# Kernel tuning notes

Hardware: AMD Instinct MI355X
Metric: run time of the kernel (lower is better)

The kernel has to match this reference:

```python
import jax, jax.numpy as jnp
import numpy as np

# Production dims: NTU-RGB+D skeletons, mid-network AGCN block
N, C, T, V = 64, 64, 300, 25   # batch, channels, frames, joints
S = 3                          # num_subset (spatial partitions of adjacency)
IC = 64 // 4                   # inter_channels = out_channels // coff_embedding
OC = 64                        # out_channels (== in_channels -> down is Identity)
BN_EPS = 1e-5


def setup_inputs() -> dict:
    key = jax.random.key(0)
    ks = jax.random.split(key, 13)
    x = jax.random.normal(ks[0], (N, C, T, V), jnp.float32)
    A = jax.random.uniform(ks[1], (S, V, V), jnp.float32)          # fixed graph buffer
    PA = jax.random.normal(ks[2], (S, V, V), jnp.float32) * 1e-3   # learned adjacency (init ~1e-6)
    wa = jax.random.normal(ks[3], (S, IC, C), jnp.float32) * 0.05  # conv_a 1x1 weights
    ba = jax.random.normal(ks[4], (S, IC), jnp.float32) * 0.01
    wb = jax.random.normal(ks[5], (S, IC, C), jnp.float32) * 0.05  # conv_b 1x1 weights
    bb = jax.random.normal(ks[6], (S, IC), jnp.float32) * 0.01
    wd = jax.random.normal(ks[7], (S, OC, C), jnp.float32) * 0.05  # conv_d 1x1 weights
    bd = jax.random.normal(ks[8], (S, OC), jnp.float32) * 0.01
    bn_gamma = jax.random.uniform(ks[9], (OC,), jnp.float32) + 0.5
    bn_beta = jax.random.normal(ks[10], (OC,), jnp.float32) * 0.1
    bn_mean = jax.random.normal(ks[11], (OC,), jnp.float32) * 0.1
    bn_var = jax.random.uniform(ks[12], (OC,), jnp.float32) + 0.5
    return {"x": x, "A": A, "PA": PA, "wa": wa, "ba": ba, "wb": wb, "bb": bb,
            "wd": wd, "bd": bd, "bn_gamma": bn_gamma, "bn_beta": bn_beta,
            "bn_mean": bn_mean, "bn_var": bn_var}


def reference(x, A, PA, wa, ba, wb, bb, wd, bd, bn_gamma, bn_beta, bn_mean, bn_var):
    n, c, t, v = x.shape
    s, ic, _ = wa.shape
    A_total = A + PA                                                # (S,V,V)

    # conv_a / conv_b are 1x1 convs over channels, vectorized over subsets
    a = jnp.einsum('nctv,skc->nsktv', x, wa) + ba[None, :, :, None, None]  # (N,S,IC,T,V)
    b = jnp.einsum('nctv,skc->nsktv', x, wb) + bb[None, :, :, None, None]

    # attention_a: permute(0,3,1,2).view(N, V, IC*T); attention_b: view(N, IC*T, V)
    a_flat = a.transpose(0, 1, 4, 2, 3).reshape(n, s, v, ic * t)   # (N,S,V,IC*T)
    b_flat = b.reshape(n, s, ic * t, v)                            # (N,S,IC*T,V)

    scores = jnp.einsum('nsvm,nsmu->nsvu', a_flat, b_flat) / (ic * t)
    att = jax.nn.softmax(scores, axis=-2) + A_total[None]          # softmax over dim -2, then + adjacency

    # feature matmul: x.view(N, C*T, V) @ att  ==  contract over node axis v
    y = jnp.einsum('nctv,nsvu->nsctu', x, att)                     # (N,S,C,T,V)
    # conv_d (1x1) per subset, summed over subsets
    z = jnp.einsum('nsctv,soc->notv', y, wd) + jnp.sum(bd, axis=0)[None, :, None, None]

    # BatchNorm2d (inference form with running stats)
    scale = (bn_gamma / jnp.sqrt(bn_var + BN_EPS))[None, :, None, None]
    zn = (z - bn_mean[None, :, None, None]) * scale + bn_beta[None, :, None, None]

    # down is Identity since in_channels == out_channels
    return jax.nn.relu(zn + x)
```

## Files before the change

kernel.cpp:

```cpp
#include <hip/hip_runtime.h>
#include <math.h>


typedef short  short4v  __attribute__((ext_vector_type(4)));
typedef short  short8v  __attribute__((ext_vector_type(8)));
typedef unsigned short ushort4v __attribute__((ext_vector_type(4)));
typedef float  float4v  __attribute__((ext_vector_type(4)));

#define MFMA_BF16(a,b,c) __builtin_amdgcn_mfma_f32_16x16x32_bf16((a),(b),(c),0,0,0)

__device__ __forceinline__ unsigned short f2bf(float f) {
  union { float f; unsigned int u; } v; v.f = f;
  unsigned int r = v.u + 0x7FFFu + ((v.u >> 16) & 1u);
  return (unsigned short)(r >> 16);
}
__device__ __forceinline__ short8v ld8_b64(const unsigned short* p) {
  short4v a = *(const short4v*)p;
  short4v b = *(const short4v*)(p + 4);
  short8v r;
  r[0]=a[0]; r[1]=a[1]; r[2]=a[2]; r[3]=a[3];
  r[4]=b[0]; r[5]=b[1]; r[6]=b[2]; r[7]=b[3];
  return r;
}

__global__ __launch_bounds__(128) void k1_scores(
    const float* __restrict__ x,  const float* __restrict__ wa,
    const float* __restrict__ ba, const float* __restrict__ wb,
    const float* __restrict__ bb, float* __restrict__ part)
{
  __shared__ __align__(16) unsigned short ET[3][160*40];
  __shared__ float biasL[96];
  const unsigned tid  = threadIdx.x;
  const unsigned lane = tid & 63u, w = tid >> 6;
  const unsigned l15  = lane & 15u, q = lane >> 4;
  const unsigned n = blockIdx.y, ts = blockIdx.x;
  const unsigned t0 = ts * 30u;
  const float* xn = x + (size_t)n * 480000;

  for (unsigned i = tid; i < 96; i += 128) {
    unsigned s = i >> 5, r = i & 31u;
    biasL[i] = (r < 16) ? ba[s*16 + r] : bb[s*16 + (r-16)];
  }

  short8v Wf[3][2][2];
  #pragma unroll
  for (int s = 0; s < 3; ++s)
    #pragma unroll
    for (int mt = 0; mt < 2; ++mt)
      #pragma unroll
      for (int ks = 0; ks < 2; ++ks) {
        unsigned kr = mt*16 + l15;
        unsigned c0 = ks*32 + q*8;
        const float* src = (kr < 16) ? (wa + ((size_t)s*16 + kr)*64 + c0)
                                     : (wb + ((size_t)s*16 + (kr-16))*64 + c0);
        short8v f;
        #pragma unroll
        for (int j = 0; j < 8; ++j) f[j] = (short)f2bf(src[j]);
        Wf[s][mt][ks] = f;
      }

  float4v acc[6];
  #pragma unroll
  for (int j = 0; j < 6; ++j) acc[j] = (float4v){0.f,0.f,0.f,0.f};

  __syncthreads();

  for (unsigned ch = 0; ch < 5; ++ch) {
    const unsigned tvbase = (t0 + ch*6u) * 25u;
    for (unsigned nn = 0; nn < 5; ++nn) {
      unsigned nt  = w + 2*nn;
      unsigned tvb = nt*16 + l15;
      unsigned tvg = tvbase + tvb;
      if (tvg > 7499u) tvg = 7499u;
      short8v B0, B1;
      #pragma unroll
      for (int j = 0; j < 8; ++j) {
        B0[j] = (short)f2bf(xn[(size_t)(q*8 + (unsigned)j)*7500 + tvg]);
        B1[j] = (short)f2bf(xn[(size_t)(32 + q*8 + (unsigned)j)*7500 + tvg]);
      }
      #pragma unroll
      for (int s = 0; s < 3; ++s)
        #pragma unroll
        for (int mt = 0; mt < 2; ++mt) {
          float4v d = (float4v){0.f,0.f,0.f,0.f};
          d = MFMA_BF16(Wf[s][mt][0], B0, d);
          d = MFMA_BF16(Wf[s][mt][1], B1, d);
          unsigned krb = mt*16 + q*4;
          ushort4v pk;
          #pragma unroll
          for (int r = 0; r < 4; ++r) pk[r] = f2bf(d[r] + biasL[s*32 + krb + r]);
          *(ushort4v*)(&ET[s][tvb*40 + krb]) = pk;
        }
    }
    __syncthreads();
    #pragma unroll
    for (int j = 0; j < 6; ++j) {
      unsigned g = (unsigned)j*2 + w;
      unsigned s = g >> 2, mt = (g >> 1) & 1u, nt2 = g & 1u;
      #pragma unroll
      for (int ks = 0; ks < 3; ++ks) {
        unsigned t    = 2*ks + (q >> 1);
        unsigned kofs = 8*(q & 1u);
        short8v Af = *(const short8v*)(&ET[s][(t*25 + mt*16  + l15)*40 + kofs]);
        short8v Bf = *(const short8v*)(&ET[s][(t*25 + nt2*16 + l15)*40 + 16 + kofs]);
        acc[j] = MFMA_BF16(Af, Bf, acc[j]);
      }
    }
    __syncthreads();
  }
  #pragma unroll
  for (int j = 0; j < 6; ++j) {
    unsigned g = (unsigned)j*2 + w;
    unsigned s = g >> 2, mt = (g >> 1) & 1u, nt2 = g & 1u;
    unsigned u = nt2*16 + l15;
    if (u < 25) {
      #pragma unroll
      for (int r = 0; r < 4; ++r) {
        unsigned v = mt*16 + q*4 + (unsigned)r;
        if (v < 25)
          part[(((size_t)ts*64 + n)*3 + s)*625 + v*25 + u] = acc[j][r];
      }
    }
  }
}

__global__ __launch_bounds__(256) void k2_softmax(
    const float* __restrict__ part, const float* __restrict__ A,
    const float* __restrict__ PA, float* __restrict__ att)
{
  __shared__ float Sc[625];
  const unsigned tid = threadIdx.x, s = blockIdx.x, n = blockIdx.y;
  for (unsigned i = tid; i < 625; i += 256) {
    float sum = 0.f;
    #pragma unroll
    for (unsigned ts = 0; ts < 10; ++ts)
      sum += part[(((size_t)ts*64 + n)*3 + s)*625 + i];
    Sc[i] = sum * (1.f/4800.f);
  }
  __syncthreads();
  if (tid < 25) {
    unsigned u = tid;
    float col[25];
    float m = -1e30f;
    #pragma unroll
    for (int v = 0; v < 25; ++v) { col[v] = Sc[(unsigned)v*25 + u]; m = fmaxf(m, col[v]); }
    float S = 0.f;
    #pragma unroll
    for (int v = 0; v < 25; ++v) { col[v] = expf(col[v] - m); S += col[v]; }
    float inv = 1.f / S;
    #pragma unroll
    for (int v = 0; v < 25; ++v)
      att[(((size_t)n*3 + s)*25 + (unsigned)v)*25 + u] =
          col[v]*inv + A[s*625 + (unsigned)v*25 + u] + PA[s*625 + (unsigned)v*25 + u];
  }
}

__global__ __launch_bounds__(256) void k3_main(
    const float* __restrict__ x,   const float* __restrict__ wd,
    const float* __restrict__ bd,  const float* __restrict__ gam,
    const float* __restrict__ bet, const float* __restrict__ mu,
    const float* __restrict__ var, const float* __restrict__ att,
    float* __restrict__ out)
{
  __shared__ __align__(16) unsigned short Pt[32*196];
  __shared__ float KS[64], KB[64];
  const unsigned tid  = threadIdx.x;
  const unsigned lane = tid & 63u, mt = tid >> 6;
  const unsigned l15  = lane & 15u, q = lane >> 4;
  const unsigned n = blockIdx.y, t0 = blockIdx.x * 30u;

  if (tid < 64) {
    float sc = gam[tid] * rsqrtf(var[tid] + 1e-5f);
    KS[tid] = sc;
    KB[tid] = (bd[tid] + bd[64+tid] + bd[128+tid] - mu[tid]) * sc + bet[tid];
  }
  short8v ATf[3][2];
  #pragma unroll
  for (int s = 0; s < 3; ++s)
    #pragma unroll
    for (int nt2 = 0; nt2 < 2; ++nt2) {
      unsigned u = (unsigned)nt2*16 + l15;
      short8v f;
      #pragma unroll
      for (int j = 0; j < 8; ++j) {
        unsigned v = q*8 + (unsigned)j;
        float a = (v < 25 && u < 25)
                ? att[(((size_t)n*3 + s)*25 + v)*25 + u] : 0.f;
        f[j] = (short)f2bf(a);
      }
      ATf[s][nt2] = f;
    }
  short8v Awf[6];
  #pragma unroll
  for (int ks = 0; ks < 6; ++ks) {
    unsigned s  = (unsigned)ks >> 1;
    unsigned c0 = ((unsigned)ks & 1u)*32 + q*8;
    const float* src = wd + ((size_t)s*64 + mt*16 + l15)*64 + c0;
    short8v f;
    #pragma unroll
    for (int j = 0; j < 8; ++j) f[j] = (short)f2bf(src[j]);
    Awf[ks] = f;
  }
  __syncthreads();

  const float* xn = x + (size_t)n * 480000;
  const float* xr = xn + (size_t)(mt*16 + l15)*7500;
  for (unsigned t = 0; t < 30; ++t) {
    const unsigned tg = t0 + t;
    const unsigned base = tg*25 + q*8;
    short8v Ax;
    #pragma unroll
    for (int j = 0; j < 8; ++j) {
      unsigned idx = base + (unsigned)j;
      if (idx > 7499u) idx = 7499u;
      Ax[j] = (short)f2bf(xr[idx]);
    }
    #pragma unroll
    for (int s = 0; s < 3; ++s)
      #pragma unroll
      for (int nt2 = 0; nt2 < 2; ++nt2) {
        float4v d = (float4v){0.f,0.f,0.f,0.f};
        d = MFMA_BF16(Ax, ATf[s][nt2], d);
        unsigned u  = (unsigned)nt2*16 + l15;
        unsigned kb = (unsigned)s*64 + mt*16 + q*4;
        ushort4v pk;
        #pragma unroll
        for (int r = 0; r < 4; ++r) pk[r] = f2bf(d[r]);
        *(ushort4v*)(&Pt[u*196 + kb]) = pk;
      }
    __syncthreads();
    float4v za = (float4v){0.f,0.f,0.f,0.f}, zb = (float4v){0.f,0.f,0.f,0.f};
    #pragma unroll
    for (int ks = 0; ks < 6; ++ks) {
      short8v B0 = ld8_b64(&Pt[l15*196      + (unsigned)ks*32 + q*8]);
      short8v B1 = ld8_b64(&Pt[(16+l15)*196 + (unsigned)ks*32 + q*8]);
      za = MFMA_BF16(Awf[ks], B0, za);
      zb = MFMA_BF16(Awf[ks], B1, zb);
    }
    #pragma unroll
    for (int nt2 = 0; nt2 < 2; ++nt2) {
      float4v zz = nt2 ? zb : za;
      unsigned u = (unsigned)nt2*16 + l15;
      if (u < 25) {
        #pragma unroll
        for (int r = 0; r < 4; ++r) {
          unsigned o = mt*16 + q*4 + (unsigned)r;
          float xv = xn[(size_t)o*7500 + tg*25 + u];
          float val = zz[r]*KS[o] + KB[o] + xv;
          out[((size_t)n*64 + o)*7500 + (size_t)tg*25 + u] = fmaxf(val, 0.f);
        }
      }
    }
    __syncthreads();
  }
}

extern "C" void kernel_launch(void* const* d_in, const int* in_sizes, int n_in,
                              void* d_out, int out_size, void* d_ws, size_t ws_size,
                              hipStream_t stream)
{
  (void)in_sizes; (void)n_in; (void)out_size; (void)ws_size;
  const float* x   = (const float*)d_in[0];
  const float* A   = (const float*)d_in[1];
  const float* PA  = (const float*)d_in[2];
  const float* wa  = (const float*)d_in[3];
  const float* ba  = (const float*)d_in[4];
  const float* wb  = (const float*)d_in[5];
  const float* bb  = (const float*)d_in[6];
  const float* wd  = (const float*)d_in[7];
  const float* bd  = (const float*)d_in[8];
  const float* gam = (const float*)d_in[9];
  const float* bet = (const float*)d_in[10];
  const float* mu  = (const float*)d_in[11];
  const float* var = (const float*)d_in[12];
  float* out  = (float*)d_out;
  float* part = (float*)d_ws;
  float* att  = part + 1200000;

  hipLaunchKernelGGL(k1_scores, dim3(10, 64), dim3(128), 0, stream,
                     x, wa, ba, wb, bb, part);
  hipLaunchKernelGGL(k2_softmax, dim3(3, 64), dim3(256), 0, stream,
                     part, A, PA, att);
  hipLaunchKernelGGL(k3_main, dim3(10, 64), dim3(256), 0, stream,
                     x, wd, bd, gam, bet, mu, var, att, out);
}
```

Before: 390.2 us.

## Raise grid parallelism, reduce scores with atomics, double-buffer main kernel

The scores kernel now splits time into 25 chunks of 12 frames with 4 waves per block. It accumulates straight into a zeroed scores buffer with atomicAdd, which removes the 10-way partial-sum pass from the softmax kernel. The main kernel uses 30 time blocks of 10 frames and double-buffers the shared Pt tile, computing the next frame's x·att product while the current frame's conv_d runs, and prefetches the residual x. This adds a zeroing launch and atomic contention, and float atomics make the summation order nondeterministic.

```diff
diff --git a/kernel.cpp b/kernel.cpp
--- a/kernel.cpp
+++ b/kernel.cpp
@@ -23,10 +23,15 @@
   return r;
 }
 
-__global__ __launch_bounds__(128) void k1_scores(
+__global__ __launch_bounds__(256) void k0_zero(float* __restrict__ p, int nelem) {
+  int i = blockIdx.x * 256 + threadIdx.x;
+  if (i < nelem) p[i] = 0.f;
+}
+
+__global__ __launch_bounds__(256) void k1_scores(
     const float* __restrict__ x,  const float* __restrict__ wa,
     const float* __restrict__ ba, const float* __restrict__ wb,
-    const float* __restrict__ bb, float* __restrict__ part)
+    const float* __restrict__ bb, float* __restrict__ scores)
 {
   __shared__ __align__(16) unsigned short ET[3][160*40];
   __shared__ float biasL[96];
@@ -34,10 +39,10 @@
   const unsigned lane = tid & 63u, w = tid >> 6;
   const unsigned l15  = lane & 15u, q = lane >> 4;
   const unsigned n = blockIdx.y, ts = blockIdx.x;
-  const unsigned t0 = ts * 30u;
+  const unsigned t0 = ts * 12u;
   const float* xn = x + (size_t)n * 480000;
 
-  for (unsigned i = tid; i < 96; i += 128) {
+  for (unsigned i = tid; i < 96; i += 256) {
     unsigned s = i >> 5, r = i & 31u;
     biasL[i] = (r < 16) ? ba[s*16 + r] : bb[s*16 + (r-16)];
   }
@@ -59,43 +64,46 @@
         Wf[s][mt][ks] = f;
       }
 
-  float4v acc[6];
-  #pragma unroll
-  for (int j = 0; j < 6; ++j) acc[j] = (float4v){0.f,0.f,0.f,0.f};
+  float4v acc[3];
+  #pragma unroll
+  for (int j = 0; j < 3; ++j) acc[j] = (float4v){0.f,0.f,0.f,0.f};
 
   __syncthreads();
 
-  for (unsigned ch = 0; ch < 5; ++ch) {
+  for (unsigned ch = 0; ch < 2; ++ch) {
     const unsigned tvbase = (t0 + ch*6u) * 25u;
-    for (unsigned nn = 0; nn < 5; ++nn) {
-      unsigned nt  = w + 2*nn;
-      unsigned tvb = nt*16 + l15;
-      unsigned tvg = tvbase + tvb;
-      if (tvg > 7499u) tvg = 7499u;
-      short8v B0, B1;
-      #pragma unroll
-      for (int j = 0; j < 8; ++j) {
-        B0[j] = (short)f2bf(xn[(size_t)(q*8 + (unsigned)j)*7500 + tvg]);
-        B1[j] = (short)f2bf(xn[(size_t)(32 + q*8 + (unsigned)j)*7500 + tvg]);
-      }
-      #pragma unroll
-      for (int s = 0; s < 3; ++s)
-        #pragma unroll
-        for (int mt = 0; mt < 2; ++mt) {
-          float4v d = (float4v){0.f,0.f,0.f,0.f};
-          d = MFMA_BF16(Wf[s][mt][0], B0, d);
-          d = MFMA_BF16(Wf[s][mt][1], B1, d);
-          unsigned krb = mt*16 + q*4;
-          ushort4v pk;
+    if (ch) __syncthreads();
+    for (unsigned nn = 0; nn < 3; ++nn) {
+      unsigned nt = w + 4*nn;
+      if (nt < 10) {
+        unsigned tvb = nt*16 + l15;
+        unsigned tvg = tvbase + tvb;
+        if (tvg > 7499u) tvg = 7499u;
+        short8v B0, B1;
+        #pragma unroll
+        for (int j = 0; j < 8; ++j) {
+          B0[j] = (short)f2bf(xn[(size_t)(q*8 + (unsigned)j)*7500 + tvg]);
+          B1[j] = (short)f2bf(xn[(size_t)(32 + q*8 + (unsigned)j)*7500 + tvg]);
+        }
+        #pragma unroll
+        for (int s = 0; s < 3; ++s)
           #pragma unroll
-          for (int r = 0; r < 4; ++r) pk[r] = f2bf(d[r] + biasL[s*32 + krb + r]);
-          *(ushort4v*)(&ET[s][tvb*40 + krb]) = pk;
-        }
+          for (int mt = 0; mt < 2; ++mt) {
+            float4v d = (float4v){0.f,0.f,0.f,0.f};
+            d = MFMA_BF16(Wf[s][mt][0], B0, d);
+            d = MFMA_BF16(Wf[s][mt][1], B1, d);
+            unsigned krb = mt*16 + q*4;
+            ushort4v pk;
+            #pragma unroll
+            for (int r = 0; r < 4; ++r) pk[r] = f2bf(d[r] + biasL[s*32 + krb + r]);
+            *(ushort4v*)(&ET[s][tvb*40 + krb]) = pk;
+          }
+      }
     }
     __syncthreads();
     #pragma unroll
-    for (int j = 0; j < 6; ++j) {
-      unsigned g = (unsigned)j*2 + w;
+    for (int j = 0; j < 3; ++j) {
+      unsigned g = (unsigned)j*4 + w;
       unsigned s = g >> 2, mt = (g >> 1) & 1u, nt2 = g & 1u;
       #pragma unroll
       for (int ks = 0; ks < 3; ++ks) {
@@ -106,11 +114,10 @@
         acc[j] = MFMA_BF16(Af, Bf, acc[j]);
       }
     }
-    __syncthreads();
-  }
-  #pragma unroll
-  for (int j = 0; j < 6; ++j) {
-    unsigned g = (unsigned)j*2 + w;
+  }
+  #pragma unroll
+  for (int j = 0; j < 3; ++j) {
+    unsigned g = (unsigned)j*4 + w;
     unsigned s = g >> 2, mt = (g >> 1) & 1u, nt2 = g & 1u;
     unsigned u = nt2*16 + l15;
     if (u < 25) {
@@ -118,41 +125,34 @@
       for (int r = 0; r < 4; ++r) {
         unsigned v = mt*16 + q*4 + (unsigned)r;
         if (v < 25)
-          part[(((size_t)ts*64 + n)*3 + s)*625 + v*25 + u] = acc[j][r];
-      }
-    }
-  }
-}
-
-__global__ __launch_bounds__(256) void k2_softmax(
-    const float* __restrict__ part, const float* __restrict__ A,
+          atomicAdd(&scores[(size_t)n*1875 + s*625 + v*25 + u], acc[j][r]);
+      }
+    }
+  }
+}
+
+__global__ __launch_bounds__(64) void k2_softmax(
+    const float* __restrict__ scores, const float* __restrict__ A,
     const float* __restrict__ PA, float* __restrict__ att)
 {
-  __shared__ float Sc[625];
   const unsigned tid = threadIdx.x, s = blockIdx.x, n = blockIdx.y;
-  for (unsigned i = tid; i < 625; i += 256) {
-    float sum = 0.f;
-    #pragma unroll
-    for (unsigned ts = 0; ts < 10; ++ts)
-      sum += part[(((size_t)ts*64 + n)*3 + s)*625 + i];
-    Sc[i] = sum * (1.f/4800.f);
-  }
-  __syncthreads();
-  if (tid < 25) {
-    unsigned u = tid;
-    float col[25];
-    float m = -1e30f;
-    #pragma unroll
-    for (int v = 0; v < 25; ++v) { col[v] = Sc[(unsigned)v*25 + u]; m = fmaxf(m, col[v]); }
-    float S = 0.f;
-    #pragma unroll
-    for (int v = 0; v < 25; ++v) { col[v] = expf(col[v] - m); S += col[v]; }
-    float inv = 1.f / S;
-    #pragma unroll
-    for (int v = 0; v < 25; ++v)
-      att[(((size_t)n*3 + s)*25 + (unsigned)v)*25 + u] =
-          col[v]*inv + A[s*625 + (unsigned)v*25 + u] + PA[s*625 + (unsigned)v*25 + u];
-  }
+  if (tid >= 25) return;
+  const unsigned u = tid;
+  float col[25];
+  float m = -1e30f;
+  #pragma unroll
+  for (int v = 0; v < 25; ++v) {
+    col[v] = scores[(size_t)n*1875 + s*625 + (unsigned)v*25 + u] * (1.f/4800.f);
+    m = fmaxf(m, col[v]);
+  }
+  float S = 0.f;
+  #pragma unroll
+  for (int v = 0; v < 25; ++v) { col[v] = expf(col[v] - m); S += col[v]; }
+  float inv = 1.f / S;
+  #pragma unroll
+  for (int v = 0; v < 25; ++v)
+    att[(((size_t)n*3 + s)*25 + (unsigned)v)*25 + u] =
+        col[v]*inv + A[s*625 + (unsigned)v*25 + u] + PA[s*625 + (unsigned)v*25 + u];
 }
 
 __global__ __launch_bounds__(256) void k3_main(
@@ -162,12 +162,12 @@
     const float* __restrict__ var, const float* __restrict__ att,
     float* __restrict__ out)
 {
-  __shared__ __align__(16) unsigned short Pt[32*196];
+  __shared__ __align__(16) unsigned short Pt[2][32*196];
   __shared__ float KS[64], KB[64];
   const unsigned tid  = threadIdx.x;
   const unsigned lane = tid & 63u, mt = tid >> 6;
   const unsigned l15  = lane & 15u, q = lane >> 4;
-  const unsigned n = blockIdx.y, t0 = blockIdx.x * 30u;
+  const unsigned n = blockIdx.y, t0 = blockIdx.x * 10u;
 
   if (tid < 64) {
     float sc = gam[tid] * rsqrtf(var[tid] + 1e-5f);
@@ -201,13 +201,12 @@
     for (int j = 0; j < 8; ++j) f[j] = (short)f2bf(src[j]);
     Awf[ks] = f;
   }
-  __syncthreads();
 
   const float* xn = x + (size_t)n * 480000;
   const float* xr = xn + (size_t)(mt*16 + l15)*7500;
-  for (unsigned t = 0; t < 30; ++t) {
-    const unsigned tg = t0 + t;
-    const unsigned base = tg*25 + q*8;
+
+  {
+    const unsigned base = t0*25 + q*8;
     short8v Ax;
     #pragma unroll
     for (int j = 0; j < 8; ++j) {
@@ -226,16 +225,56 @@
         ushort4v pk;
         #pragma unroll
         for (int r = 0; r < 4; ++r) pk[r] = f2bf(d[r]);
-        *(ushort4v*)(&Pt[u*196 + kb]) = pk;
-      }
+        *(ushort4v*)(&Pt[0][u*196 + kb]) = pk;
+      }
+  }
+
+  for (unsigned t = 0; t < 10; ++t) {
+    const unsigned cur = t & 1u, nxt = cur ^ 1u;
+    const unsigned tg = t0 + t;
     __syncthreads();
+
+    const bool hasnext = (t + 1u < 10u);
+    short8v Axn;
+    if (hasnext) {
+      const unsigned base = (tg + 1u)*25 + q*8;
+      #pragma unroll
+      for (int j = 0; j < 8; ++j) Axn[j] = (short)f2bf(xr[base + (unsigned)j]);
+    }
+    float xv[2][4];
+    #pragma unroll
+    for (int nt2 = 0; nt2 < 2; ++nt2) {
+      unsigned u = (unsigned)nt2*16 + l15;
+      if (u < 25) {
+        #pragma unroll
+        for (int r = 0; r < 4; ++r) {
+          unsigned o = mt*16 + q*4 + (unsigned)r;
+          xv[nt2][r] = xn[(size_t)o*7500 + tg*25 + u];
+        }
+      }
+    }
     float4v za = (float4v){0.f,0.f,0.f,0.f}, zb = (float4v){0.f,0.f,0.f,0.f};
     #pragma unroll
     for (int ks = 0; ks < 6; ++ks) {
-      short8v B0 = ld8_b64(&Pt[l15*196      + (unsigned)ks*32 + q*8]);
-      short8v B1 = ld8_b64(&Pt[(16+l15)*196 + (unsigned)ks*32 + q*8]);
+      short8v B0 = ld8_b64(&Pt[cur][l15*196      + (unsigned)ks*32 + q*8]);
+      short8v B1 = ld8_b64(&Pt[cur][(16+l15)*196 + (unsigned)ks*32 + q*8]);
       za = MFMA_BF16(Awf[ks], B0, za);
       zb = MFMA_BF16(Awf[ks], B1, zb);
+    }
+    if (hasnext) {
+      #pragma unroll
+      for (int s = 0; s < 3; ++s)
+        #pragma unroll
+        for (int nt2 = 0; nt2 < 2; ++nt2) {
+          float4v d = (float4v){0.f,0.f,0.f,0.f};
+          d = MFMA_BF16(Axn, ATf[s][nt2], d);
+          unsigned u  = (unsigned)nt2*16 + l15;
+          unsigned kb = (unsigned)s*64 + mt*16 + q*4;
+          ushort4v pk;
+          #pragma unroll
+          for (int r = 0; r < 4; ++r) pk[r] = f2bf(d[r]);
+          *(ushort4v*)(&Pt[nxt][u*196 + kb]) = pk;
+        }
     }
     #pragma unroll
     for (int nt2 = 0; nt2 < 2; ++nt2) {
@@ -245,13 +284,11 @@
         #pragma unroll
         for (int r = 0; r < 4; ++r) {
           unsigned o = mt*16 + q*4 + (unsigned)r;
-          float xv = xn[(size_t)o*7500 + tg*25 + u];
-          float val = zz[r]*KS[o] + KB[o] + xv;
+          float val = zz[r]*KS[o] + KB[o] + xv[nt2][r];
           out[((size_t)n*64 + o)*7500 + (size_t)tg*25 + u] = fmaxf(val, 0.f);
         }
       }
     }
-    __syncthreads();
   }
 }
 
@@ -273,14 +310,16 @@
   const float* bet = (const float*)d_in[10];
   const float* mu  = (const float*)d_in[11];
   const float* var = (const float*)d_in[12];
-  float* out  = (float*)d_out;
-  float* part = (float*)d_ws;
-  float* att  = part + 1200000;
-
-  hipLaunchKernelGGL(k1_scores, dim3(10, 64), dim3(128), 0, stream,
-                     x, wa, ba, wb, bb, part);
-  hipLaunchKernelGGL(k2_softmax, dim3(3, 64), dim3(256), 0, stream,
-                     part, A, PA, att);
-  hipLaunchKernelGGL(k3_main, dim3(10, 64), dim3(256), 0, stream,
+  float* out    = (float*)d_out;
+  float* scores = (float*)d_ws;
+  float* att    = scores + 120000;
+
+  hipLaunchKernelGGL(k0_zero, dim3((120000 + 255)/256), dim3(256), 0, stream,
+                     scores, 120000);
+  hipLaunchKernelGGL(k1_scores, dim3(25, 64), dim3(256), 0, stream,
+                     x, wa, ba, wb, bb, scores);
+  hipLaunchKernelGGL(k2_softmax, dim3(3, 64), dim3(64), 0, stream,
+                     scores, A, PA, att);
+  hipLaunchKernelGGL(k3_main, dim3(30, 64), dim3(256), 0, stream,
                      x, wd, bd, gam, bet, mu, var, att, out);
 }
```

Result: no change. 383.6 us (-1.7%).
